# Performance work log

Hardware: AMD Instinct MI355X
Metric: run time of the kernel (lower is better)

Reference implementation:

```python
import jax, jax.numpy as jnp
import numpy as np
from jax import lax


def conv2d(x, w, b, pad):
    y = lax.conv_general_dilated(x, w, (1, 1), [(pad, pad), (pad, pad)],
                                 dimension_numbers=('NCHW', 'OIHW', 'NCHW'))
    return y + b[None, :, None, None]


def grid_sample_bilinear_border(img, grid):
    # img [B,C,H,W], grid [B,h,w,2] normalized to [-1,1] (x,y), align_corners=False
    B, C, H, W = img.shape
    gx, gy = grid[..., 0], grid[..., 1]
    ix = jnp.clip(((gx + 1.0) * W - 1.0) * 0.5, 0.0, W - 1.0)  # border padding = clamp coords
    iy = jnp.clip(((gy + 1.0) * H - 1.0) * 0.5, 0.0, H - 1.0)
    x0f, y0f = jnp.floor(ix), jnp.floor(iy)
    wx, wy = ix - x0f, iy - y0f                       # [B,h,w]
    x0 = jnp.clip(x0f.astype(jnp.int32), 0, W - 1)
    y0 = jnp.clip(y0f.astype(jnp.int32), 0, H - 1)
    x1 = jnp.clip(x0 + 1, 0, W - 1)
    y1 = jnp.clip(y0 + 1, 0, H - 1)
    gather = jax.vmap(lambda im, yi, xi: im[:, yi, xi])  # -> [B,C,h,w]
    v00 = gather(img, y0, x0)
    v01 = gather(img, y0, x1)
    v10 = gather(img, y1, x0)
    v11 = gather(img, y1, x1)
    wx, wy = wx[:, None], wy[:, None]                  # [B,1,h,w]
    return (v00 * (1 - wx) * (1 - wy) + v01 * wx * (1 - wy)
            + v10 * (1 - wx) * wy + v11 * wx * wy)


def setup_inputs():
    key = jax.random.key(0)
    ks = jax.random.split(key, 16)
    B, Ch, H, W = 8, 256, 64, 64
    Cl, h, w = 128, 128, 128
    Co, r = 128, 8
    s = 0.05
    return {
        'f_high': jax.random.normal(ks[0], (B, Ch, H, W), jnp.float32),
        'f_low': jax.random.normal(ks[1], (B, Cl, h, w), jnp.float32),
        'off_w1': jax.random.normal(ks[2], (64, Ch + Cl, 3, 3), jnp.float32) * s,
        'off_b1': jnp.zeros((64,), jnp.float32),
        'off_w2': jax.random.normal(ks[3], (2, 64, 3, 3), jnp.float32) * s,
        'off_b2': jnp.zeros((2,), jnp.float32),
        'proj_w': jax.random.normal(ks[4], (Co, Ch), jnp.float32) * s,
        'proj_b': jnp.zeros((Co,), jnp.float32),
        'ca_w1': jax.random.normal(ks[5], (Co // r, Co), jnp.float32) * s,
        'ca_b1': jnp.zeros((Co // r,), jnp.float32),
        'ca_w2': jax.random.normal(ks[6], (Co, Co // r), jnp.float32) * s,
        'ca_b2': jnp.zeros((Co,), jnp.float32),
        'sa_w': jax.random.normal(ks[7], (1, 2, 7, 7), jnp.float32) * s,
        'sa_b': jnp.zeros((1,), jnp.float32),
    }


def reference(f_high, f_low, off_w1, off_b1, off_w2, off_b2,
              proj_w, proj_b, ca_w1, ca_b1, ca_w2, ca_b2, sa_w, sa_b):
    B, Ch, H, W = f_high.shape
    _, Cl, h, w = f_low.shape
    # resize f_high to (h,w) (bilinear, half-pixel centers == align_corners=False)
    fh_r = jax.image.resize(f_high, (B, Ch, h, w), 'bilinear', antialias=False)
    cat = jnp.concatenate([fh_r, f_low], axis=1)       # [B,Ch+Cl,h,w]
    hid = jax.nn.relu(conv2d(cat, off_w1, off_b1, 1))
    offset = conv2d(hid, off_w2, off_b2, 1)            # [B,2,h,w]
    # base normalized grid (x,y) in [-1,1]
    ys = jnp.linspace(-1.0, 1.0, h, dtype=f_high.dtype)
    xs = jnp.linspace(-1.0, 1.0, w, dtype=f_high.dtype)
    gy, gx = jnp.meshgrid(ys, xs, indexing='ij')
    base = jnp.stack([gx, gy], axis=-1)[None]          # [1,h,w,2]
    scale = jnp.array([2.0 / w, 2.0 / h], dtype=f_high.dtype)
    grid = base + offset.transpose(0, 2, 3, 1) * scale  # [B,h,w,2]
    f_aligned = grid_sample_bilinear_border(f_high, grid)  # [B,Ch,h,w]
    # 1x1 proj Ch -> Co
    x = jnp.einsum('oc,bchw->bohw', proj_w, f_aligned) + proj_b[None, :, None, None]
    # multi-attention fusion: channel (SE) then spatial (CBAM-style)
    p = x.mean(axis=(2, 3))                            # [B,Co]
    a = jax.nn.sigmoid(jax.nn.relu(p @ ca_w1.T + ca_b1) @ ca_w2.T + ca_b2)
    xc = x * a[:, :, None, None]
    sm = jnp.concatenate([xc.mean(axis=1, keepdims=True),
                          xc.max(axis=1, keepdims=True)], axis=1)  # [B,2,h,w]
    sa = jax.nn.sigmoid(conv2d(sm, sa_w, sa_b, 3))
    return xc * sa
```

## Files before the change

### kernel.cpp

```cpp
#include <hip/hip_runtime.h>
#include <hip/hip_fp16.h>
#include <math.h>

typedef _Float16 f16;
typedef _Float16 f16x8 __attribute__((ext_vector_type(8)));
typedef _Float16 f16x2 __attribute__((ext_vector_type(2)));
typedef float f32x4 __attribute__((ext_vector_type(4)));

__device__ __forceinline__ void gll16(const void* g, void* l) {
  __builtin_amdgcn_global_load_lds((const __attribute__((address_space(1))) void*)g,
                                   (__attribute__((address_space(3))) void*)l, 16, 0, 0);
}

__global__ __launch_bounds__(256) void pack_conv_w(const float* __restrict__ w,
                                                   f16* __restrict__ out,
                                                   int CIN, int MFR, int COUT) {
  int idx = blockIdx.x * 256 + threadIdx.x;
  int KC = CIN / 32;
  int total = 9 * KC * MFR * 64 * 8;
  if (idx >= total) return;
  int j = idx & 7;
  int lane = (idx >> 3) & 63;
  int rest = idx >> 9;
  int mf = rest % MFR; rest /= MFR;
  int kc = rest % KC; int t = rest / KC;
  int oc = mf * 16 + (lane & 15);
  int c = kc * 32 + (lane >> 4) * 8 + j;
  int ky = t / 3, kx = t % 3;
  float v = (oc < COUT) ? w[((oc * CIN + c) * 3 + ky) * 3 + kx] : 0.f;
  out[idx] = (f16)v;
}

__global__ __launch_bounds__(256) void pack_proj_w(const float* __restrict__ w,
                                                   f16* __restrict__ out) {
  int idx = blockIdx.x * 256 + threadIdx.x;
  int j = idx & 7; int lane = (idx >> 3) & 63; int rest = idx >> 9;
  int mf = rest & 7; int kc = rest >> 3;
  int oc = mf * 16 + (lane & 15);
  int c = kc * 32 + (lane >> 4) * 8 + j;
  out[idx] = (f16)w[oc * 256 + c];
}

__global__ __launch_bounds__(256) void k_zero(f16* __restrict__ cat, f16* __restrict__ hid) {
  int idx = blockIdx.x * 256 + threadIdx.x;
  f16x8 z = {(f16)0, (f16)0, (f16)0, (f16)0, (f16)0, (f16)0, (f16)0, (f16)0};
  int p, b, c8;
  f16* dst; int C;
  if (idx < 198144) {
    c8 = idx % 48; int rest = idx / 48; p = rest % 516; b = rest / 516;
    dst = cat; C = 384;
  } else {
    int i2 = idx - 198144;
    c8 = i2 % 8; int rest = i2 / 8; p = rest % 516; b = rest / 516;
    dst = hid; C = 64;
  }
  int y, x;
  if (p < 130) { y = 0; x = p; }
  else if (p < 260) { y = 129; x = p - 130; }
  else if (p < 388) { y = p - 260 + 1; x = 0; }
  else { y = p - 388 + 1; x = 129; }
  *(f16x8*)&dst[(((size_t)b * 130 + y) * 130 + x) * C + c8 * 8] = z;
}

__global__ __launch_bounds__(256) void k_fhw(const float* __restrict__ fh,
                                             f16* __restrict__ fhw) {
  __shared__ float lds[128 * 17];
  int wg = blockIdx.x;
  int xt = wg & 3; int ch2 = (wg >> 2) & 1; int y = (wg >> 3) & 63; int b = wg >> 9;
  int x0 = xt * 16;
  int tid = threadIdx.x;
  for (int i = 0; i < 8; ++i) {
    int u = i * 256 + tid;
    int c = u >> 4, xi = u & 15;
    lds[c * 17 + xi] = fh[(((size_t)b * 256 + ch2 * 128 + c) * 64 + y) * 64 + x0 + xi];
  }
  __syncthreads();
  {
    int x = tid >> 4, cl = tid & 15;
    f16x8 v;
    #pragma unroll
    for (int j = 0; j < 8; ++j) v[j] = (f16)lds[(cl * 8 + j) * 17 + x];
    int coct = ch2 * 16 + cl;
    *(f16x8*)&fhw[(((size_t)b * 64 + y) * 64 + x0 + x) * 256 + coct * 8] = v;
  }
}

__global__ __launch_bounds__(256) void k_catA(const f16* __restrict__ fhw,
                                              f16* __restrict__ cat) {
  int wg = blockIdx.x;
  int Y = wg & 127, b = wg >> 7;
  float iy = fminf(fmaxf(Y * 0.5f - 0.25f, 0.f), 63.f);
  int y0 = (int)iy; float wy = iy - y0; int y1 = min(y0 + 1, 63);
  int tid = threadIdx.x;
  for (int i = 0; i < 16; ++i) {
    int u = i * 256 + tid; int X = u >> 5, coct = u & 31;
    float ix = fminf(fmaxf(X * 0.5f - 0.25f, 0.f), 63.f);
    int x0 = (int)ix; float wx = ix - x0; int x1 = min(x0 + 1, 63);
    f16x8 v00 = *(const f16x8*)&fhw[(((size_t)b * 64 + y0) * 64 + x0) * 256 + coct * 8];
    f16x8 v01 = *(const f16x8*)&fhw[(((size_t)b * 64 + y0) * 64 + x1) * 256 + coct * 8];
    f16x8 v10 = *(const f16x8*)&fhw[(((size_t)b * 64 + y1) * 64 + x0) * 256 + coct * 8];
    f16x8 v11 = *(const f16x8*)&fhw[(((size_t)b * 64 + y1) * 64 + x1) * 256 + coct * 8];
    f16x8 r;
    #pragma unroll
    for (int j = 0; j < 8; ++j) {
      float t0 = (1.f - wx) * (float)v00[j] + wx * (float)v01[j];
      float t1 = (1.f - wx) * (float)v10[j] + wx * (float)v11[j];
      r[j] = (f16)((1.f - wy) * t0 + wy * t1);
    }
    *(f16x8*)&cat[(((size_t)b * 130 + 1 + Y) * 130 + 1 + X) * 384 + coct * 8] = r;
  }
}

__global__ __launch_bounds__(256) void k_catB(const float* __restrict__ fl,
                                              f16* __restrict__ cat) {
  __shared__ float lds[128 * 17];
  int wg = blockIdx.x;
  int xt = wg & 7; int Y = (wg >> 3) & 127; int b = wg >> 10;
  int x0 = xt * 16; int tid = threadIdx.x;
  for (int i = 0; i < 8; ++i) {
    int u = i * 256 + tid; int c = u >> 4, xi = u & 15;
    lds[c * 17 + xi] = fl[(((size_t)b * 128 + c) * 128 + Y) * 128 + x0 + xi];
  }
  __syncthreads();
  {
    int x = tid >> 4, coct = tid & 15;
    f16x8 v;
    #pragma unroll
    for (int j = 0; j < 8; ++j) v[j] = (f16)lds[(coct * 8 + j) * 17 + x];
    *(f16x8*)&cat[(((size_t)b * 130 + 1 + Y) * 130 + 1 + x0 + x) * 384 + 256 + coct * 8] = v;
  }
}

template<int CIN, int MFR, int COUT, bool RELU, int OPAD>
__global__ __launch_bounds__(256, 2) void k_conv3(const f16* __restrict__ in,
                                                  const f16* __restrict__ apack,
                                                  const float* __restrict__ bias,
                                                  f16* __restrict__ out) {
  constexpr int KC = CIN / 32;
  constexpr int PATCH = 21504;
  __shared__ __align__(16) char ldsb[2 * PATCH];
  int wg = blockIdx.x;
  int tx = wg & 7, ty = (wg >> 3) & 7, b = wg >> 6;
  int y0 = ty * 16, x0 = tx * 16;
  int tid = threadIdx.x, lane = tid & 63, w = tid >> 6;
  int lx = lane & 15, hi = lane >> 4, w4 = w * 4;

  int ro[6];
  #pragma unroll
  for (int j = 0; j < 6; ++j) {
    int s = j * 256 + w * 64 + lane;
    if (s > 1295) s = 1295;
    int p = s >> 2, coct = s & 3;
    int py = p / 18, px = p % 18;
    int cocts = coct ^ ((px >> 1) & 3);
    ro[j] = ((y0 + py) * 130 + (x0 + px)) * CIN + cocts * 8;
  }
  const f16* inb = in + (size_t)b * 130 * 130 * CIN;

  f32x4 acc[MFR][4];
  #pragma unroll
  for (int m = 0; m < MFR; ++m)
    #pragma unroll
    for (int n = 0; n < 4; ++n) acc[m][n] = (f32x4){0.f, 0.f, 0.f, 0.f};

  auto stage = [&](int kc, int buf) {
    #pragma unroll
    for (int j = 0; j < 6; ++j) {
      if (j < 5 || w == 0) {
        gll16(inb + ro[j] + kc * 32, ldsb + buf * PATCH + (j * 256 + w * 64) * 16);
      }
    }
  };

  stage(0, 0);
  __syncthreads();
  for (int kc = 0; kc < KC; ++kc) {
    if (kc + 1 < KC) stage(kc + 1, (kc + 1) & 1);
    const char* cb = ldsb + (kc & 1) * PATCH;
    __builtin_amdgcn_s_setprio(1);
    #pragma unroll
    for (int kx = 0; kx < 3; ++kx) {
      int px = lx + kx;
      int sw = (px >> 1) & 3;
      f16x8 bf[6];
      #pragma unroll
      for (int s = 0; s < 6; ++s) {
        int slot = ((w4 + s) * 18 + px) * 4 + (hi ^ sw);
        bf[s] = *(const f16x8*)(cb + slot * 16);
      }
      #pragma unroll
      for (int ky = 0; ky < 3; ++ky) {
        f16x8 af[MFR];
        #pragma unroll
        for (int m = 0; m < MFR; ++m)
          af[m] = *(const f16x8*)&apack[(size_t)((((ky * 3 + kx) * KC + kc) * MFR + m) * 64 + lane) * 8];
        #pragma unroll
        for (int n = 0; n < 4; ++n)
          #pragma unroll
          for (int m = 0; m < MFR; ++m)
            acc[m][n] = __builtin_amdgcn_mfma_f32_16x16x32_f16(af[m], bf[n + ky], acc[m][n], 0, 0, 0);
      }
    }
    __builtin_amdgcn_s_setprio(0);
    __syncthreads();
  }

  constexpr int S = 128 + 2 * OPAD;
  #pragma unroll
  for (int m = 0; m < MFR; ++m)
    #pragma unroll
    for (int n = 0; n < 4; ++n) {
      int pos = w * 64 + n * 16 + lx;
      #pragma unroll
      for (int rp = 0; rp < 2; ++rp) {
        int ch = m * 16 + hi * 4 + rp * 2;
        if (ch < COUT) {
          float v0 = acc[m][n][rp * 2 + 0] + bias[ch];
          float v1 = acc[m][n][rp * 2 + 1] + bias[ch + 1];
          if (RELU) { v0 = fmaxf(v0, 0.f); v1 = fmaxf(v1, 0.f); }
          f16x2 pk; pk[0] = (f16)v0; pk[1] = (f16)v1;
          int addr = ((pos * COUT + ch) * 2) ^ ((pos & 7) << 4);
          *(f16x2*)(ldsb + addr) = pk;
        }
      }
    }
  __syncthreads();
  for (int u = tid; u < 256 * COUT / 2; u += 256) {
    int pos = u / (COUT / 2); int cp = u % (COUT / 2);
    int addr = ((pos * COUT + cp * 2) * 2) ^ ((pos & 7) << 4);
    f16x2 v = *(const f16x2*)(ldsb + addr);
    int y = y0 + (pos >> 4) + OPAD, x = x0 + (pos & 15) + OPAD;
    *(f16x2*)&out[(((size_t)b * S + y) * S + x) * COUT + cp * 2] = v;
  }
}

__global__ __launch_bounds__(256) void k_gp(const f16* __restrict__ fhw,
                                            const f16* __restrict__ off,
                                            const f16* __restrict__ ppack,
                                            const float* __restrict__ pbias,
                                            f16* __restrict__ x,
                                            float* __restrict__ psum) {
  __shared__ f16 bt[64 * 256];
  __shared__ float4 samp[64];
  char* ldsb = (char*)bt;
  int wg = blockIdx.x;
  int b = wg & 7, tile = wg >> 3;
  int pbase = tile * 64;
  int tid = threadIdx.x, lane = tid & 63, w = tid >> 6;
  if (tid < 64) {
    int pos = pbase + tid;
    int yy = pos >> 7, xx = pos & 127;
    float o0 = (float)off[((size_t)b * 16384 + pos) * 2 + 0];
    float o1 = (float)off[((size_t)b * 16384 + pos) * 2 + 1];
    float gx = -1.f + xx * (2.f / 127.f) + o0 * (1.f / 64.f);
    float gy = -1.f + yy * (2.f / 127.f) + o1 * (1.f / 64.f);
    float ix = fminf(fmaxf((gx + 1.f) * 32.f - 0.5f, 0.f), 63.f);
    float iy = fminf(fmaxf((gy + 1.f) * 32.f - 0.5f, 0.f), 63.f);
    float x0f = floorf(ix), y0f = floorf(iy);
    samp[tid] = make_float4(x0f, y0f, ix - x0f, iy - y0f);
  }
  __syncthreads();
  for (int i = 0; i < 8; ++i) {
    int u = i * 256 + tid; int p = u >> 5, coct = u & 31;
    float4 s = samp[p];
    int x0i = (int)s.x, y0i = (int)s.y;
    int x1i = min(x0i + 1, 63), y1i = min(y0i + 1, 63);
    float wx = s.z, wy = s.w;
    const f16* bb = fhw + (size_t)b * 4096 * 256 + coct * 8;
    f16x8 v00 = *(const f16x8*)&bb[(y0i * 64 + x0i) * 256];
    f16x8 v01 = *(const f16x8*)&bb[(y0i * 64 + x1i) * 256];
    f16x8 v10 = *(const f16x8*)&bb[(y1i * 64 + x0i) * 256];
    f16x8 v11 = *(const f16x8*)&bb[(y1i * 64 + x1i) * 256];
    f16x8 r;
    #pragma unroll
    for (int j = 0; j < 8; ++j) {
      float t0 = (1.f - wx) * (float)v00[j] + wx * (float)v01[j];
      float t1 = (1.f - wx) * (float)v10[j] + wx * (float)v11[j];
      r[j] = (f16)((1.f - wy) * t0 + wy * t1);
    }
    int addr = (p * 512 + coct * 16) ^ ((p & 7) << 4);
    *(f16x8*)(ldsb + addr) = r;
  }
  __syncthreads();
  f32x4 acc[2][4];
  #pragma unroll
  for (int m = 0; m < 2; ++m)
    #pragma unroll
    for (int n = 0; n < 4; ++n) acc[m][n] = (f32x4){0.f, 0.f, 0.f, 0.f};
  #pragma unroll
  for (int kc = 0; kc < 8; ++kc) {
    f16x8 af[2];
    #pragma unroll
    for (int m = 0; m < 2; ++m)
      af[m] = *(const f16x8*)&ppack[(size_t)((kc * 8 + w * 2 + m) * 64 + lane) * 8];
    #pragma unroll
    for (int n = 0; n < 4; ++n) {
      int p = n * 16 + (lane & 15);
      int addr = (p * 512 + kc * 64 + ((lane >> 4) * 16)) ^ ((p & 7) << 4);
      f16x8 bf = *(const f16x8*)(ldsb + addr);
      #pragma unroll
      for (int m = 0; m < 2; ++m)
        acc[m][n] = __builtin_amdgcn_mfma_f32_16x16x32_f16(af[m], bf, acc[m][n], 0, 0, 0);
    }
  }
  __syncthreads();
  #pragma unroll
  for (int m = 0; m < 2; ++m)
    #pragma unroll
    for (int n = 0; n < 4; ++n) {
      int p = n * 16 + (lane & 15);
      #pragma unroll
      for (int r = 0; r < 4; ++r) {
        int ch = w * 32 + m * 16 + (lane >> 4) * 4 + r;
        int addr = ((p * 128 + ch) * 4) ^ ((p & 7) << 4);
        *(float*)(ldsb + addr) = acc[m][n][r];
      }
    }
  __syncthreads();
  float part0 = 0.f, part1 = 0.f;
  int cp = tid & 63, wv = tid >> 6;
  int c0 = cp * 2;
  float b0 = pbias[c0], b1 = pbias[c0 + 1];
  #pragma unroll
  for (int i = 0; i < 16; ++i) {
    int p = i * 4 + wv;
    float v0 = *(const float*)(ldsb + (((p * 128 + c0) * 4) ^ ((p & 7) << 4)));
    float v1 = *(const float*)(ldsb + (((p * 128 + c0 + 1) * 4) ^ ((p & 7) << 4)));
    v0 += b0; v1 += b1;
    f16x2 pk; pk[0] = (f16)v0; pk[1] = (f16)v1;
    *(f16x2*)&x[((size_t)b * 16384 + pbase + p) * 128 + c0] = pk;
    part0 += v0; part1 += v1;
  }
  __syncthreads();
  float* rl = (float*)ldsb;
  rl[wv * 128 + c0] = part0; rl[wv * 128 + c0 + 1] = part1;
  __syncthreads();
  if (tid < 128)
    psum[(size_t)wg * 128 + tid] = rl[tid] + rl[128 + tid] + rl[256 + tid] + rl[384 + tid];
}

__global__ __launch_bounds__(128) void k_ca(const float* __restrict__ psum,
                                            const float* __restrict__ w1, const float* __restrict__ b1,
                                            const float* __restrict__ w2, const float* __restrict__ b2,
                                            float* __restrict__ a) {
  __shared__ float pl[128];
  __shared__ float hl[16];
  int b = blockIdx.x; int tid = threadIdx.x;
  float s = 0.f;
  for (int t = 0; t < 256; ++t) s += psum[(size_t)(t * 8 + b) * 128 + tid];
  pl[tid] = s * (1.f / 16384.f);
  __syncthreads();
  if (tid < 16) {
    float h = b1[tid];
    for (int c = 0; c < 128; ++c) h += pl[c] * w1[tid * 128 + c];
    hl[tid] = fmaxf(h, 0.f);
  }
  __syncthreads();
  float z = b2[tid];
  #pragma unroll
  for (int o2 = 0; o2 < 16; ++o2) z += hl[o2] * w2[tid * 16 + o2];
  a[b * 128 + tid] = 1.f / (1.f + expf(-z));
}

__global__ __launch_bounds__(256) void k_sm(const f16* __restrict__ x,
                                            const float* __restrict__ a,
                                            float* __restrict__ meanp, float* __restrict__ maxp) {
  __shared__ float al[128];
  int wg = blockIdx.x;
  int pbase = wg * 128;
  int b = pbase >> 14;
  int tid = threadIdx.x;
  if (tid < 128) al[tid] = a[b * 128 + tid];
  __syncthreads();
  #pragma unroll
  for (int i = 0; i < 8; ++i) {
    int u = i * 256 + tid;
    int p = u >> 4, q = u & 15;
    f16x8 v = *(const f16x8*)&x[((size_t)pbase + p) * 128 + q * 8];
    float sm = 0.f, mx = -1e30f;
    #pragma unroll
    for (int j = 0; j < 8; ++j) {
      float xc = (float)v[j] * al[q * 8 + j];
      sm += xc; mx = fmaxf(mx, xc);
    }
    #pragma unroll
    for (int d = 1; d < 16; d <<= 1) {
      sm += __shfl_xor(sm, d);
      mx = fmaxf(mx, __shfl_xor(mx, d));
    }
    if ((tid & 15) == 0) {
      meanp[pbase + p] = sm * (1.f / 128.f);
      maxp[pbase + p] = mx;
    }
  }
}

__global__ __launch_bounds__(256) void k_sa(const float* __restrict__ meanp,
                                            const float* __restrict__ maxp,
                                            const float* __restrict__ sw, const float* __restrict__ sb,
                                            float* __restrict__ sap) {
  __shared__ float lds[2][22][22];
  __shared__ float wl[98];
  int wg = blockIdx.x;
  int tx = wg & 7, ty = (wg >> 3) & 7, b = wg >> 6;
  int y0 = ty * 16, x0 = tx * 16;
  int tid = threadIdx.x;
  if (tid < 98) wl[tid] = sw[tid];
  for (int u = tid; u < 2 * 22 * 22; u += 256) {
    int ch = u / 484; int p = u % 484; int py = p / 22, px = p % 22;
    int gy = y0 + py - 3, gx = x0 + px - 3;
    float v = 0.f;
    if (gy >= 0 && gy < 128 && gx >= 0 && gx < 128)
      v = ch ? maxp[(size_t)b * 16384 + gy * 128 + gx] : meanp[(size_t)b * 16384 + gy * 128 + gx];
    lds[ch][py][px] = v;
  }
  __syncthreads();
  int py = tid >> 4, px = tid & 15;
  float accv = sb[0];
  #pragma unroll
  for (int ch = 0; ch < 2; ++ch)
    for (int ky = 0; ky < 7; ++ky)
      #pragma unroll
      for (int kx = 0; kx < 7; ++kx)
        accv += lds[ch][py + ky][px + kx] * wl[ch * 49 + ky * 7 + kx];
  sap[(size_t)b * 16384 + (y0 + py) * 128 + x0 + px] = 1.f / (1.f + expf(-accv));
}

__global__ __launch_bounds__(256) void k_out(const f16* __restrict__ x,
                                             const float* __restrict__ a,
                                             const float* __restrict__ sap,
                                             float* __restrict__ out) {
  __shared__ float lds[32 * 129];
  __shared__ float al[128];
  __shared__ float sl[32];
  int wg = blockIdx.x;
  int pbase = wg * 32; int b = pbase >> 14;
  int tid = threadIdx.x;
  if (tid < 128) al[tid] = a[b * 128 + tid];
  if (tid < 32) sl[tid] = sap[pbase + tid];
  __syncthreads();
  #pragma unroll
  for (int i = 0; i < 2; ++i) {
    int u = i * 256 + tid;
    int p = u >> 4, q = u & 15;
    f16x8 v = *(const f16x8*)&x[((size_t)pbase + p) * 128 + q * 8];
    #pragma unroll
    for (int j = 0; j < 8; ++j) lds[p * 129 + q * 8 + j] = (float)v[j];
  }
  __syncthreads();
  #pragma unroll
  for (int i = 0; i < 16; ++i) {
    int u = i * 256 + tid; int c = u >> 5, p = u & 31;
    float v = lds[p * 129 + c] * al[c] * sl[p];
    out[((size_t)(b * 128 + c)) * 16384 + (pbase & 16383) + p] = v;
  }
}

extern "C" void kernel_launch(void* const* d_in, const int* in_sizes, int n_in,
                              void* d_out, int out_size, void* d_ws, size_t ws_size,
                              hipStream_t stream) {
  const float* f_high = (const float*)d_in[0];
  const float* f_low  = (const float*)d_in[1];
  const float* off_w1 = (const float*)d_in[2];
  const float* off_b1 = (const float*)d_in[3];
  const float* off_w2 = (const float*)d_in[4];
  const float* off_b2 = (const float*)d_in[5];
  const float* proj_w = (const float*)d_in[6];
  const float* proj_b = (const float*)d_in[7];
  const float* ca_w1  = (const float*)d_in[8];
  const float* ca_b1  = (const float*)d_in[9];
  const float* ca_w2  = (const float*)d_in[10];
  const float* ca_b2  = (const float*)d_in[11];
  const float* sa_w   = (const float*)d_in[12];
  const float* sa_b   = (const float*)d_in[13];
  float* out = (float*)d_out;

  char* ws = (char*)d_ws; size_t o = 0;
  auto alloc = [&](size_t b) { char* p = ws + o; o += (b + 255) & ~(size_t)255; return p; };
  f16*   fhw  = (f16*)alloc(8ull * 4096 * 256 * 2);
  f16*   cat  = (f16*)alloc(8ull * 130 * 130 * 384 * 2);
  f16*   hid  = (f16*)alloc(8ull * 130 * 130 * 64 * 2);
  f16*   offb = (f16*)alloc(8ull * 16384 * 2 * 2);
  f16*   ap1  = (f16*)alloc(221184ull * 2);
  f16*   ap2  = (f16*)alloc(9216ull * 2);
  f16*   pp   = (f16*)alloc(32768ull * 2);
  f16*   xbuf = (f16*)alloc(8ull * 16384 * 128 * 2);
  float* ps   = (float*)alloc(2048ull * 128 * 4);
  float* av   = (float*)alloc(8ull * 128 * 4);
  float* mp   = (float*)alloc(131072ull * 4);
  float* xp   = (float*)alloc(131072ull * 4);
  float* sp   = (float*)alloc(131072ull * 4);

  pack_conv_w<<<864, 256, 0, stream>>>(off_w1, ap1, 384, 4, 64);
  pack_conv_w<<<36, 256, 0, stream>>>(off_w2, ap2, 64, 1, 2);
  pack_proj_w<<<128, 256, 0, stream>>>(proj_w, pp);
  k_zero<<<903, 256, 0, stream>>>(cat, hid);
  k_fhw<<<4096, 256, 0, stream>>>(f_high, fhw);
  k_catA<<<1024, 256, 0, stream>>>(fhw, cat);
  k_catB<<<8192, 256, 0, stream>>>(f_low, cat);
  k_conv3<384, 4, 64, true, 1><<<512, 256, 0, stream>>>(cat, ap1, off_b1, hid);
  k_conv3<64, 1, 2, false, 0><<<512, 256, 0, stream>>>(hid, ap2, off_b2, offb);
  k_gp<<<2048, 256, 0, stream>>>(fhw, offb, pp, proj_b, xbuf, ps);
  k_ca<<<8, 128, 0, stream>>>(ps, ca_w1, ca_b1, ca_w2, ca_b2, av);
  k_sm<<<1024, 256, 0, stream>>>(xbuf, av, mp, xp);
  k_sa<<<512, 256, 0, stream>>>(mp, xp, sa_w, sa_b, sp);
  k_out<<<4096, 256, 0, stream>>>(xbuf, av, sp, out);
}
```

Measured before the change: 342.0 us.

## Double conv1 tile height to reuse weight fragments and vectorize epilogue stores

Templates the 3x3 MFMA conv over rows-per-wave (NR). The first conv now computes 32x16 output tiles with 8 rows per wave, so each global weight fragment load feeds twice as many MFMAs and the halo overhead per output shrinks. That conv uses 256 workgroups, and a launch-bounds variant of 1 WG/SM allows more registers and LDS. The epilogue writes 16-byte vectors when COUT is a multiple of 8. In exchange, occupancy and the number of workgroups drop (256 WGs on a 256-CU part), which may hurt latency hiding.

```diff
diff --git a/kernel.cpp b/kernel.cpp
--- a/kernel.cpp
+++ b/kernel.cpp
@@ -131,25 +131,34 @@
   }
 }
 
-template<int CIN, int MFR, int COUT, bool RELU, int OPAD>
-__global__ __launch_bounds__(256, 2) void k_conv3(const f16* __restrict__ in,
-                                                  const f16* __restrict__ apack,
-                                                  const float* __restrict__ bias,
-                                                  f16* __restrict__ out) {
+template<int CIN, int MFR, int COUT, bool RELU, int OPAD, int NR, bool FORCE1>
+__global__ __launch_bounds__(256, FORCE1 ? 1 : 2) void k_conv3(const f16* __restrict__ in,
+                                                               const f16* __restrict__ apack,
+                                                               const float* __restrict__ bias,
+                                                               f16* __restrict__ out) {
   constexpr int KC = CIN / 32;
-  constexpr int PATCH = 21504;
-  __shared__ __align__(16) char ldsb[2 * PATCH];
-  int wg = blockIdx.x;
-  int tx = wg & 7, ty = (wg >> 3) & 7, b = wg >> 6;
-  int y0 = ty * 16, x0 = tx * 16;
+  constexpr int TROWS = 4 * NR;
+  constexpr int TY = 128 / TROWS;
+  constexpr int NSLOT = (TROWS + 2) * 18 * 4;
+  constexpr int NPAD = (NSLOT + 255) & ~255;
+  constexpr int ROUNDS = NPAD / 256;
+  constexpr int PATCH = NPAD * 16;
+  constexpr int EPI = TROWS * 16 * COUT * 2;
+  constexpr int LDS_SZ = (2 * PATCH > EPI ? 2 * PATCH : EPI) + (FORCE1 ? 1024 : 0);
+  __shared__ __align__(16) char ldsb[LDS_SZ];
+  int wg = blockIdx.x;
+  int b = wg & 7; int t = wg >> 3;
+  int ty = t % TY, tx = t / TY;
+  int y0 = ty * TROWS, x0 = tx * 16;
   int tid = threadIdx.x, lane = tid & 63, w = tid >> 6;
-  int lx = lane & 15, hi = lane >> 4, w4 = w * 4;
-
-  int ro[6];
-  #pragma unroll
-  for (int j = 0; j < 6; ++j) {
+  int lx = lane & 15, hi = lane >> 4;
+  int wN = w * NR;
+
+  int ro[ROUNDS];
+  #pragma unroll
+  for (int j = 0; j < ROUNDS; ++j) {
     int s = j * 256 + w * 64 + lane;
-    if (s > 1295) s = 1295;
+    if (s > NSLOT - 1) s = NSLOT - 1;
     int p = s >> 2, coct = s & 3;
     int py = p / 18, px = p % 18;
     int cocts = coct ^ ((px >> 1) & 3);
@@ -157,19 +166,16 @@
   }
   const f16* inb = in + (size_t)b * 130 * 130 * CIN;
 
-  f32x4 acc[MFR][4];
+  f32x4 acc[MFR][NR];
   #pragma unroll
   for (int m = 0; m < MFR; ++m)
     #pragma unroll
-    for (int n = 0; n < 4; ++n) acc[m][n] = (f32x4){0.f, 0.f, 0.f, 0.f};
+    for (int n = 0; n < NR; ++n) acc[m][n] = (f32x4){0.f, 0.f, 0.f, 0.f};
 
   auto stage = [&](int kc, int buf) {
     #pragma unroll
-    for (int j = 0; j < 6; ++j) {
-      if (j < 5 || w == 0) {
-        gll16(inb + ro[j] + kc * 32, ldsb + buf * PATCH + (j * 256 + w * 64) * 16);
-      }
-    }
+    for (int j = 0; j < ROUNDS; ++j)
+      gll16(inb + ro[j] + kc * 32, ldsb + buf * PATCH + (j * 256 + w * 64) * 16);
   };
 
   stage(0, 0);
@@ -182,10 +188,10 @@
     for (int kx = 0; kx < 3; ++kx) {
       int px = lx + kx;
       int sw = (px >> 1) & 3;
-      f16x8 bf[6];
+      f16x8 bf[NR + 2];
       #pragma unroll
-      for (int s = 0; s < 6; ++s) {
-        int slot = ((w4 + s) * 18 + px) * 4 + (hi ^ sw);
+      for (int s = 0; s < NR + 2; ++s) {
+        int slot = ((wN + s) * 18 + px) * 4 + (hi ^ sw);
         bf[s] = *(const f16x8*)(cb + slot * 16);
       }
       #pragma unroll
@@ -195,7 +201,7 @@
         for (int m = 0; m < MFR; ++m)
           af[m] = *(const f16x8*)&apack[(size_t)((((ky * 3 + kx) * KC + kc) * MFR + m) * 64 + lane) * 8];
         #pragma unroll
-        for (int n = 0; n < 4; ++n)
+        for (int n = 0; n < NR; ++n)
           #pragma unroll
           for (int m = 0; m < MFR; ++m)
             acc[m][n] = __builtin_amdgcn_mfma_f32_16x16x32_f16(af[m], bf[n + ky], acc[m][n], 0, 0, 0);
@@ -209,8 +215,8 @@
   #pragma unroll
   for (int m = 0; m < MFR; ++m)
     #pragma unroll
-    for (int n = 0; n < 4; ++n) {
-      int pos = w * 64 + n * 16 + lx;
+    for (int n = 0; n < NR; ++n) {
+      int pos = (wN + n) * 16 + lx;
       #pragma unroll
       for (int rp = 0; rp < 2; ++rp) {
         int ch = m * 16 + hi * 4 + rp * 2;
@@ -225,12 +231,22 @@
       }
     }
   __syncthreads();
-  for (int u = tid; u < 256 * COUT / 2; u += 256) {
-    int pos = u / (COUT / 2); int cp = u % (COUT / 2);
-    int addr = ((pos * COUT + cp * 2) * 2) ^ ((pos & 7) << 4);
-    f16x2 v = *(const f16x2*)(ldsb + addr);
-    int y = y0 + (pos >> 4) + OPAD, x = x0 + (pos & 15) + OPAD;
-    *(f16x2*)&out[(((size_t)b * S + y) * S + x) * COUT + cp * 2] = v;
+  if constexpr (COUT % 8 == 0) {
+    for (int u = tid; u < TROWS * 16 * COUT / 8; u += 256) {
+      int pos = u / (COUT / 8); int cp = u % (COUT / 8);
+      int addr = ((pos * COUT + cp * 8) * 2) ^ ((pos & 7) << 4);
+      f16x8 v = *(const f16x8*)(ldsb + addr);
+      int y = y0 + (pos >> 4) + OPAD, x = x0 + (pos & 15) + OPAD;
+      *(f16x8*)&out[(((size_t)b * S + y) * S + x) * COUT + cp * 8] = v;
+    }
+  } else {
+    for (int u = tid; u < TROWS * 16 * COUT / 2; u += 256) {
+      int pos = u / (COUT / 2); int cp = u % (COUT / 2);
+      int addr = ((pos * COUT + cp * 2) * 2) ^ ((pos & 7) << 4);
+      f16x2 v = *(const f16x2*)(ldsb + addr);
+      int y = y0 + (pos >> 4) + OPAD, x = x0 + (pos & 15) + OPAD;
+      *(f16x2*)&out[(((size_t)b * S + y) * S + x) * COUT + cp * 2] = v;
+    }
   }
 }
 
@@ -498,8 +514,8 @@
   k_fhw<<<4096, 256, 0, stream>>>(f_high, fhw);
   k_catA<<<1024, 256, 0, stream>>>(fhw, cat);
   k_catB<<<8192, 256, 0, stream>>>(f_low, cat);
-  k_conv3<384, 4, 64, true, 1><<<512, 256, 0, stream>>>(cat, ap1, off_b1, hid);
-  k_conv3<64, 1, 2, false, 0><<<512, 256, 0, stream>>>(hid, ap2, off_b2, offb);
+  k_conv3<384, 4, 64, true, 1, 8, true><<<256, 256, 0, stream>>>(cat, ap1, off_b1, hid);
+  k_conv3<64, 1, 2, false, 0, 4, false><<<512, 256, 0, stream>>>(hid, ap2, off_b2, offb);
   k_gp<<<2048, 256, 0, stream>>>(fhw, offb, pp, proj_b, xbuf, ps);
   k_ca<<<8, 128, 0, stream>>>(ps, ca_w1, ca_b1, ca_w2, ca_b2, av);
   k_sm<<<1024, 256, 0, stream>>>(xbuf, av, mp, xp);
```

Measured after the change: 358.2 us. +4.7%, slower.
